# Optimization experiments

Hardware: AMD Instinct MI355X
Metric: run time of the kernel (lower is better)

The kernel has to match this reference:

```python
import jax, jax.numpy as jnp
import numpy as np

HEAD_DIM = 64
EMBED_DIM = 1024


def setup_inputs() -> dict:
    key = jax.random.key(0)
    k0, k1, k2, k3, k4, k5, k6 = jax.random.split(key, 7)
    B, T = 4, 2048
    s = 1.0 / np.sqrt(EMBED_DIM)
    return {
        "inputs": jax.random.normal(k0, (B, T, EMBED_DIM), dtype=jnp.float32),
        "Wq": jax.random.uniform(k1, (HEAD_DIM, EMBED_DIM), jnp.float32, -s, s),
        "bq": jax.random.uniform(k2, (HEAD_DIM,), jnp.float32, -s, s),
        "Wk": jax.random.uniform(k3, (HEAD_DIM, EMBED_DIM), jnp.float32, -s, s),
        "bk": jax.random.uniform(k4, (HEAD_DIM,), jnp.float32, -s, s),
        "Wv": jax.random.uniform(k5, (HEAD_DIM, EMBED_DIM), jnp.float32, -s, s),
        "bv": jax.random.uniform(k6, (HEAD_DIM,), jnp.float32, -s, s),
    }


def reference(inputs, Wq, bq, Wk, bk, Wv, bv):
    # inputs: [B, T, E]
    q = jnp.einsum("bte,he->bth", inputs, Wq) + bq  # [B, T, H]
    k = jnp.einsum("bte,he->bth", inputs, Wk) + bk
    v = jnp.einsum("bte,he->bth", inputs, Wv) + bv
    scores = jnp.einsum("bth,bsh->bts", q, k)  # [B, T, T]
    T = scores.shape[-1]
    causal = jnp.tril(jnp.ones((T, T), dtype=bool))  # True = keep
    scores = jnp.where(causal, scores, -jnp.inf)
    weights = jax.nn.softmax(scores / jnp.sqrt(jnp.float32(HEAD_DIM)), axis=-1)
    # dropout is identity in eval mode
    return jnp.einsum("bts,bsh->bth", weights, v)
```

## Files before the change

kernel.cpp:

```cpp
#include <hip/hip_runtime.h>
#include <hip/hip_bf16.h>

#define BATCH 4
#define SEQ   2048
#define EMB   1024
#define HD    64
#define BT    (BATCH * SEQ)
#define XS_STRIDE 1040

#define QSCALE 0.18033688011112042f

typedef __attribute__((ext_vector_type(8))) short bf16x8;
typedef __attribute__((ext_vector_type(4))) float f32x4;

__device__ __forceinline__ ushort f2bf(float f) {
    unsigned u = __float_as_uint(f);
    return (ushort)((u + 0x7FFFu + ((u >> 16) & 1u)) >> 16);
}

__global__ __launch_bounds__(256) void prep(
    const float* __restrict__ Wq, const float* __restrict__ bq,
    const float* __restrict__ Wk, const float* __restrict__ bk,
    const float* __restrict__ Wv, const float* __restrict__ bv,
    ushort* __restrict__ Wf, float* __restrict__ bb)
{
    const int fid = (int)blockIdx.x * 256 + (int)threadIdx.x;
    const int kc   = fid / 768;
    const int rem  = fid - kc * 768;
    const int sub  = rem >> 6;
    const int lane = rem & 63;
    const int row  = (sub & 3) * 16 + (lane & 15);
    const int e0   = kc * 32 + (lane >> 4) * 8;
    const float* W = (sub < 4) ? Wq : ((sub < 8) ? Wk : Wv);
    const float4 a0 = *(const float4*)(W + (size_t)row * EMB + e0);
    const float4 a1 = *(const float4*)(W + (size_t)row * EMB + e0 + 4);
    bf16x8 w;
    w[0] = (short)f2bf(a0.x); w[1] = (short)f2bf(a0.y);
    w[2] = (short)f2bf(a0.z); w[3] = (short)f2bf(a0.w);
    w[4] = (short)f2bf(a1.x); w[5] = (short)f2bf(a1.y);
    w[6] = (short)f2bf(a1.z); w[7] = (short)f2bf(a1.w);
    *(bf16x8*)(Wf + (size_t)fid * 8) = w;
    if (blockIdx.x == 0 && threadIdx.x < 192) {
        const int i = (int)threadIdx.x;
        const float* B = (i < 64) ? bq : ((i < 128) ? bk : bv);
        bb[i] = B[i & 63];
    }
}

__global__ __launch_bounds__(512, 2) void qkv_gemm(
    const float* __restrict__ x, const ushort* __restrict__ Wf,
    const float* __restrict__ bb,
    ushort* __restrict__ Qf, ushort* __restrict__ Kf, ushort* __restrict__ Vf)
{
    const int t0   = (int)blockIdx.x * 32;
    const int tid  = (int)threadIdx.x;
    const int wv   = tid >> 6;
    const int lane = tid & 63;
    const int col  = lane & 15, quad = lane >> 4;
    const int sg   = wv >> 1;
    const int kp   = wv & 1;
    const int sub0 = sg * 3;

    __shared__ ushort xs[32][XS_STRIDE];
    __shared__ __align__(16) float red[4][64][24];

    float4 v0[8];
    #pragma unroll
    for (int i = 0; i < 8; ++i) {
        const int idx = i * 512 + tid;
        const int row = idx >> 7, c4 = idx & 127;
        v0[i] = *(const float4*)(x + (size_t)(t0 + row) * EMB + c4 * 4);
    }
    #pragma unroll
    for (int i = 0; i < 8; ++i) {
        const int idx = i * 512 + tid;
        const int row = idx >> 7, c4 = idx & 127;
        ushort4 pk;
        pk.x = f2bf(v0[i].x); pk.y = f2bf(v0[i].y);
        pk.z = f2bf(v0[i].z); pk.w = f2bf(v0[i].w);
        *(ushort4*)&xs[row][c4 * 4] = pk;
    }
    __syncthreads();

    float4 v1[8];
    #pragma unroll
    for (int i = 0; i < 8; ++i) {
        const int idx = i * 512 + tid;
        const int row = idx >> 7, c4 = idx & 127;
        v1[i] = *(const float4*)(x + (size_t)(t0 + row) * EMB + 512 + c4 * 4);
    }

    f32x4 acc[2][3];
    #pragma unroll
    for (int rg = 0; rg < 2; ++rg)
        #pragma unroll
        for (int s = 0; s < 3; ++s) acc[rg][s] = (f32x4){0.f, 0.f, 0.f, 0.f};

    #pragma unroll 4
    for (int t = 0; t < 8; ++t) {
        const int kc = kp + 2 * t;
        const bf16x8 a0 = *(const bf16x8*)&xs[col][kc * 32 + quad * 8];
        const bf16x8 a1 = *(const bf16x8*)&xs[16 + col][kc * 32 + quad * 8];
        #pragma unroll
        for (int s = 0; s < 3; ++s) {
            const bf16x8 w = *(const bf16x8*)(Wf + ((size_t)(kc * 12 + sub0 + s) * 64 + lane) * 8);
            acc[0][s] = __builtin_amdgcn_mfma_f32_16x16x32_bf16(a0, w, acc[0][s], 0, 0, 0);
            acc[1][s] = __builtin_amdgcn_mfma_f32_16x16x32_bf16(a1, w, acc[1][s], 0, 0, 0);
        }
    }

    #pragma unroll
    for (int i = 0; i < 8; ++i) {
        const int idx = i * 512 + tid;
        const int row = idx >> 7, c4 = idx & 127;
        ushort4 pk;
        pk.x = f2bf(v1[i].x); pk.y = f2bf(v1[i].y);
        pk.z = f2bf(v1[i].z); pk.w = f2bf(v1[i].w);
        *(ushort4*)&xs[row][512 + c4 * 4] = pk;
    }
    __syncthreads();

    #pragma unroll 4
    for (int t = 0; t < 8; ++t) {
        const int kc = 16 + kp + 2 * t;
        const bf16x8 a0 = *(const bf16x8*)&xs[col][kc * 32 + quad * 8];
        const bf16x8 a1 = *(const bf16x8*)&xs[16 + col][kc * 32 + quad * 8];
        #pragma unroll
        for (int s = 0; s < 3; ++s) {
            const bf16x8 w = *(const bf16x8*)(Wf + ((size_t)(kc * 12 + sub0 + s) * 64 + lane) * 8);
            acc[0][s] = __builtin_amdgcn_mfma_f32_16x16x32_bf16(a0, w, acc[0][s], 0, 0, 0);
            acc[1][s] = __builtin_amdgcn_mfma_f32_16x16x32_bf16(a1, w, acc[1][s], 0, 0, 0);
        }
    }

    if (kp) {
        #pragma unroll
        for (int rg = 0; rg < 2; ++rg)
            #pragma unroll
            for (int s = 0; s < 3; ++s)
                *(f32x4*)&red[sg][lane][(rg * 3 + s) * 4] = acc[rg][s];
    }
    __syncthreads();
    if (kp) return;
    #pragma unroll
    for (int rg = 0; rg < 2; ++rg)
        #pragma unroll
        for (int s = 0; s < 3; ++s)
            acc[rg][s] += *(const f32x4*)&red[sg][lane][(rg * 3 + s) * 4];

    #pragma unroll
    for (int rg = 0; rg < 2; ++rg) {
        const int tt0 = t0 + rg * 16;
        const int b   = tt0 >> 11;
        const int qt  = (tt0 >> 4) & 127;
        const int sgt = tt0 + quad * 4;
        const int itk = (sgt & (SEQ - 1)) >> 6;
        #pragma unroll
        for (int s = 0; s < 3; ++s) {
            const int sub  = sub0 + s;
            const int hrow = sub * 16 + col;
            const float bias = bb[hrow];
            if (sub < 4) {
                const int h = hrow;
                const int f = h >> 5, qd = (h >> 3) & 3, jj = h & 7;
                ushort* base = Qf + (((size_t)(b * 128 + qt) * 2 + f) * 64 + qd * 16 + quad * 4) * 8 + jj;
                #pragma unroll
                for (int i = 0; i < 4; ++i)
                    base[i * 8] = f2bf((acc[rg][s][i] + bias) * QSCALE);
            } else if (sub < 8) {
                const int h = hrow - 64;
                const int f = h >> 5, qd = (h >> 3) & 3, jj = h & 7;
                const size_t frag = ((size_t)(b * 32 + itk) * 4 + ((sgt >> 4) & 3)) * 2 + f;
                ushort* base = Kf + frag * 512 + ((size_t)((sgt & 15) + 16 * qd)) * 8 + jj;
                #pragma unroll
                for (int i = 0; i < 4; ++i)
                    base[i * 8] = f2bf(acc[rg][s][i] + bias);
            } else {
                const int h = hrow - 128;
                const int k0 = sgt & 63;
                const int f = k0 >> 5, qd = (k0 >> 3) & 3, j0 = k0 & 7;
                const size_t frag = ((size_t)(b * 32 + itk) * 4 + (h >> 4)) * 2 + f;
                ushort4 pk;
                pk.x = f2bf(acc[rg][s][0] + bias); pk.y = f2bf(acc[rg][s][1] + bias);
                pk.z = f2bf(acc[rg][s][2] + bias); pk.w = f2bf(acc[rg][s][3] + bias);
                *(ushort4*)(Vf + frag * 512 + ((size_t)((h & 15) + 16 * qd)) * 8 + j0) = pk;
            }
        }
    }
}

__global__ __launch_bounds__(512, 2) void attn(
    const ushort* __restrict__ Qf, const ushort* __restrict__ Kf,
    const ushort* __restrict__ Vf, float* __restrict__ out)
{
    const int blk  = (int)blockIdx.x;
    const int b    = blk & 3;
    const int tl   = 63 - (blk >> 2);
    const int t0   = tl * 32;
    const int nt   = ((t0 + 31) >> 6) + 1;
    const int tid  = (int)threadIdx.x;
    const int j    = tid >> 6;
    const int lane = tid & 63;
    const int col  = lane & 15, quad = lane >> 4;

    const ushort* QbA = Qf + ((size_t)(b * 128 + 2 * tl) * 2) * 512;
    const bf16x8 aqA0 = *(const bf16x8*)(QbA + (size_t)lane * 8);
    const bf16x8 aqA1 = *(const bf16x8*)(QbA + 512 + (size_t)lane * 8);
    const bf16x8 aqB0 = *(const bf16x8*)(QbA + 1024 + (size_t)lane * 8);
    const bf16x8 aqB1 = *(const bf16x8*)(QbA + 1536 + (size_t)lane * 8);

    float l_a[4], l_b[4];
    f32x4 o[8];
    #pragma unroll
    for (int i = 0; i < 4; ++i) { l_a[i] = 0.f; l_b[i] = 0.f; }
    #pragma unroll
    for (int i = 0; i < 8; ++i) o[i] = (f32x4){0.f, 0.f, 0.f, 0.f};

    __shared__ ushort pt[8][32][80];
    __shared__ __align__(16) float op[8][32][68];
    __shared__ float ll[8][32];

    bf16x8 kc[4][2];
    if (j < nt) {
        const ushort* Kt = Kf + ((size_t)(b * 32 + j) * 8) * 512;
        #pragma unroll
        for (int sub = 0; sub < 4; ++sub) {
            kc[sub][0] = *(const bf16x8*)(Kt + (size_t)(sub * 2 + 0) * 512 + (size_t)lane * 8);
            kc[sub][1] = *(const bf16x8*)(Kt + (size_t)(sub * 2 + 1) * 512 + (size_t)lane * 8);
        }
    }

    for (int it = j; it < nt; it += 8) {
        const int s0 = it * 64;
        const bool hasNext = (it + 8 < nt);

        f32x4 scA[4], scB[4];
        #pragma unroll
        for (int sub = 0; sub < 4; ++sub) {
            f32x4 z = {0.f, 0.f, 0.f, 0.f};
            z = __builtin_amdgcn_mfma_f32_16x16x32_bf16(aqA0, kc[sub][0], z, 0, 0, 0);
            z = __builtin_amdgcn_mfma_f32_16x16x32_bf16(aqA1, kc[sub][1], z, 0, 0, 0);
            scA[sub] = z;
            f32x4 y = {0.f, 0.f, 0.f, 0.f};
            y = __builtin_amdgcn_mfma_f32_16x16x32_bf16(aqB0, kc[sub][0], y, 0, 0, 0);
            y = __builtin_amdgcn_mfma_f32_16x16x32_bf16(aqB1, kc[sub][1], y, 0, 0, 0);
            scB[sub] = y;
        }

        bf16x8 kn[4][2], vf[4][2];
        {
            const ushort* Vt = Vf + ((size_t)(b * 32 + it) * 8) * 512;
            #pragma unroll
            for (int sub = 0; sub < 4; ++sub) {
                vf[sub][0] = *(const bf16x8*)(Vt + (size_t)(sub * 2 + 0) * 512 + (size_t)lane * 8);
                vf[sub][1] = *(const bf16x8*)(Vt + (size_t)(sub * 2 + 1) * 512 + (size_t)lane * 8);
            }
        }
        if (hasNext) {
            const ushort* Kt = Kf + ((size_t)(b * 32 + it + 8) * 8) * 512;
            #pragma unroll
            for (int sub = 0; sub < 4; ++sub) {
                kn[sub][0] = *(const bf16x8*)(Kt + (size_t)(sub * 2 + 0) * 512 + (size_t)lane * 8);
                kn[sub][1] = *(const bf16x8*)(Kt + (size_t)(sub * 2 + 1) * 512 + (size_t)lane * 8);
            }
        }

        if (it == nt - 1) {
            #pragma unroll
            for (int sub = 0; sub < 4; ++sub)
                #pragma unroll
                for (int i = 0; i < 4; ++i) {
                    const int s  = s0 + sub * 16 + col;
                    const int tA = t0 + quad * 4 + i;
                    if (s > tA)      scA[sub][i] = -1e30f;
                    if (s > tA + 16) scB[sub][i] = -1e30f;
                }
        }

        #pragma unroll
        for (int sub = 0; sub < 4; ++sub)
            #pragma unroll
            for (int i = 0; i < 4; ++i) {
                const float pA = exp2f(scA[sub][i]);
                l_a[i] += pA;
                pt[j][quad * 4 + i][sub * 16 + col] = f2bf(pA);
                const float pB = exp2f(scB[sub][i]);
                l_b[i] += pB;
                pt[j][16 + quad * 4 + i][sub * 16 + col] = f2bf(pB);
            }

        __asm__ volatile("s_waitcnt lgkmcnt(0)" ::: "memory");
        const bf16x8 apA0 = *(const bf16x8*)&pt[j][col][quad * 8];
        const bf16x8 apA1 = *(const bf16x8*)&pt[j][col][32 + quad * 8];
        const bf16x8 apB0 = *(const bf16x8*)&pt[j][16 + col][quad * 8];
        const bf16x8 apB1 = *(const bf16x8*)&pt[j][16 + col][32 + quad * 8];

        #pragma unroll
        for (int sub = 0; sub < 4; ++sub) {
            o[sub]     = __builtin_amdgcn_mfma_f32_16x16x32_bf16(apA0, vf[sub][0], o[sub], 0, 0, 0);
            o[sub]     = __builtin_amdgcn_mfma_f32_16x16x32_bf16(apA1, vf[sub][1], o[sub], 0, 0, 0);
            o[4 + sub] = __builtin_amdgcn_mfma_f32_16x16x32_bf16(apB0, vf[sub][0], o[4 + sub], 0, 0, 0);
            o[4 + sub] = __builtin_amdgcn_mfma_f32_16x16x32_bf16(apB1, vf[sub][1], o[4 + sub], 0, 0, 0);
        }

        if (hasNext) {
            #pragma unroll
            for (int sub = 0; sub < 4; ++sub) { kc[sub][0] = kn[sub][0]; kc[sub][1] = kn[sub][1]; }
        }
    }

    #pragma unroll
    for (int d = 1; d < 16; d <<= 1)
        #pragma unroll
        for (int i = 0; i < 4; ++i) {
            l_a[i] += __shfl_xor(l_a[i], d, 64);
            l_b[i] += __shfl_xor(l_b[i], d, 64);
        }

    #pragma unroll
    for (int sub = 0; sub < 4; ++sub)
        #pragma unroll
        for (int i = 0; i < 4; ++i) {
            op[j][quad * 4 + i][sub * 16 + col]      = o[sub][i];
            op[j][16 + quad * 4 + i][sub * 16 + col] = o[4 + sub][i];
        }
    if (col == 0) {
        #pragma unroll
        for (int i = 0; i < 4; ++i) {
            ll[j][quad * 4 + i]      = l_a[i];
            ll[j][16 + quad * 4 + i] = l_b[i];
        }
    }
    __syncthreads();

    {
        const int row = tid >> 4, c0 = (tid & 15) * 4;
        float sx = 0.f, sy = 0.f, sz = 0.f, sw = 0.f, ls = 0.f;
        #pragma unroll
        for (int w = 0; w < 8; ++w) {
            const float4 p = *(const float4*)&op[w][row][c0];
            sx += p.x; sy += p.y; sz += p.z; sw += p.w;
            ls += ll[w][row];
        }
        const float rinv = 1.0f / ls;
        float4 res;
        res.x = sx * rinv; res.y = sy * rinv; res.z = sz * rinv; res.w = sw * rinv;
        *(float4*)(out + ((size_t)b * SEQ + t0 + row) * HD + c0) = res;
    }
}

extern "C" void kernel_launch(void* const* d_in, const int* in_sizes, int n_in,
                              void* d_out, int out_size, void* d_ws, size_t ws_size,
                              hipStream_t stream)
{
    const float* x  = (const float*)d_in[0];
    const float* Wq = (const float*)d_in[1];
    const float* bq = (const float*)d_in[2];
    const float* Wk = (const float*)d_in[3];
    const float* bk = (const float*)d_in[4];
    const float* Wv = (const float*)d_in[5];
    const float* bv = (const float*)d_in[6];
    float* out = (float*)d_out;

    char* ws = (char*)d_ws;
    ushort* Wf  = (ushort*)(ws);
    float*  bb  = (float*)(ws + 0x60000);
    ushort* Qfb = (ushort*)(ws + 0x61000);
    ushort* Kfb = (ushort*)(ws + 0x161000);
    ushort* Vfb = (ushort*)(ws + 0x261000);

    prep<<<96, 256, 0, stream>>>(Wq, bq, Wk, bk, Wv, bv, Wf, bb);
    qkv_gemm<<<BT / 32, 512, 0, stream>>>(x, Wf, bb, Qfb, Kfb, Vfb);
    attn<<<256, 512, 0, stream>>>(Qfb, Kfb, Vfb, out);
}
```

Baseline: 105.1 us.

## Split attention into 64-row query tiles with causal KV chunking and atomic combine

The attention kernel now gives each block 64 query rows instead of 32. The key range is split into chunks of up to 8 KV tiles, spread over 320 blocks, and each warp handles exactly one KV tile. Partial outputs and row sums go to a workspace, and the last-arriving block for each query tile, found with an atomic counter, combines them. The goal is to balance the causal triangle across blocks and to double Q reuse per K/V load, at the cost of a large shared buffer (about 136KB, which limits occupancy to one block per CU), extra global partial traffic, and the loss of the K prefetch loop.

Result: slower. 208.2 us (+98.1%).

```diff
diff --git a/kernel.cpp b/kernel.cpp
--- a/kernel.cpp
+++ b/kernel.cpp
@@ -22,7 +22,7 @@
     const float* __restrict__ Wq, const float* __restrict__ bq,
     const float* __restrict__ Wk, const float* __restrict__ bk,
     const float* __restrict__ Wv, const float* __restrict__ bv,
-    ushort* __restrict__ Wf, float* __restrict__ bb)
+    ushort* __restrict__ Wf, float* __restrict__ bb, uint* __restrict__ cnt)
 {
     const int fid = (int)blockIdx.x * 256 + (int)threadIdx.x;
     const int kc   = fid / 768;
@@ -45,6 +45,7 @@
         const float* B = (i < 64) ? bq : ((i < 128) ? bk : bv);
         bb[i] = B[i & 63];
     }
+    if (blockIdx.x == 1 && threadIdx.x < 128) cnt[threadIdx.x] = 0u;
 }
 
 __global__ __launch_bounds__(512, 2) void qkv_gemm(
@@ -191,161 +192,185 @@
 
 __global__ __launch_bounds__(512, 2) void attn(
     const ushort* __restrict__ Qf, const ushort* __restrict__ Kf,
-    const ushort* __restrict__ Vf, float* __restrict__ out)
+    const ushort* __restrict__ Vf, float* __restrict__ part,
+    uint* __restrict__ cnt, float* __restrict__ out)
 {
-    const int blk  = (int)blockIdx.x;
-    const int b    = blk & 3;
-    const int tl   = 63 - (blk >> 2);
-    const int t0   = tl * 32;
-    const int nt   = ((t0 + 31) >> 6) + 1;
+    const int u = (int)blockIdx.x;
+    int b, tl, chunk, chunks;
+    if (u < 128)      { const int q = u >> 2;                   b = q >> 3; tl = 24 + (q & 7); chunk = u & 3;     chunks = 4; }
+    else if (u < 224) { const int v = u - 128; const int q = v / 3; b = q >> 3; tl = 16 + (q & 7); chunk = v - q * 3; chunks = 3; }
+    else if (u < 288) { const int v = u - 224; const int q = v >> 1; b = q >> 3; tl = 8 + (q & 7);  chunk = v & 1;     chunks = 2; }
+    else              { const int v = u - 288;                  b = v >> 3; tl = v & 7;        chunk = 0;         chunks = 1; }
+
+    const int t0   = tl * 64;
+    const int nt   = tl + 1;
     const int tid  = (int)threadIdx.x;
     const int j    = tid >> 6;
     const int lane = tid & 63;
     const int col  = lane & 15, quad = lane >> 4;
-
-    const ushort* QbA = Qf + ((size_t)(b * 128 + 2 * tl) * 2) * 512;
-    const bf16x8 aqA0 = *(const bf16x8*)(QbA + (size_t)lane * 8);
-    const bf16x8 aqA1 = *(const bf16x8*)(QbA + 512 + (size_t)lane * 8);
-    const bf16x8 aqB0 = *(const bf16x8*)(QbA + 1024 + (size_t)lane * 8);
-    const bf16x8 aqB1 = *(const bf16x8*)(QbA + 1536 + (size_t)lane * 8);
-
-    float l_a[4], l_b[4];
-    f32x4 o[8];
-    #pragma unroll
-    for (int i = 0; i < 4; ++i) { l_a[i] = 0.f; l_b[i] = 0.f; }
-    #pragma unroll
-    for (int i = 0; i < 8; ++i) o[i] = (f32x4){0.f, 0.f, 0.f, 0.f};
-
-    __shared__ ushort pt[8][32][80];
-    __shared__ __align__(16) float op[8][32][68];
-    __shared__ float ll[8][32];
-
-    bf16x8 kc[4][2];
-    if (j < nt) {
-        const ushort* Kt = Kf + ((size_t)(b * 32 + j) * 8) * 512;
+    const int it   = chunk * 8 + j;
+    const bool active = (it < nt);
+
+    __shared__ __align__(16) char smem[139264];
+    ushort (*pt)[64][80] = (ushort (*)[64][80])smem;
+    float  (*op)[64][68] = (float  (*)[64][68])smem;
+    __shared__ float ll[8][64];
+    __shared__ int flag;
+
+    f32x4 o[4][4];
+    float l_r[16];
+    #pragma unroll
+    for (int qs = 0; qs < 4; ++qs)
+        #pragma unroll
+        for (int d = 0; d < 4; ++d) o[qs][d] = (f32x4){0.f, 0.f, 0.f, 0.f};
+    #pragma unroll
+    for (int k = 0; k < 16; ++k) l_r[k] = 0.f;
+
+    if (active) {
+        const ushort* Qb = Qf + ((size_t)(b * 128 + tl * 4) * 2) * 512;
+        bf16x8 aq[4][2];
+        #pragma unroll
+        for (int qs = 0; qs < 4; ++qs) {
+            aq[qs][0] = *(const bf16x8*)(Qb + (size_t)(qs * 2 + 0) * 512 + (size_t)lane * 8);
+            aq[qs][1] = *(const bf16x8*)(Qb + (size_t)(qs * 2 + 1) * 512 + (size_t)lane * 8);
+        }
+        const ushort* Kt = Kf + ((size_t)(b * 32 + it) * 8) * 512;
+        bf16x8 kc[4][2];
         #pragma unroll
         for (int sub = 0; sub < 4; ++sub) {
             kc[sub][0] = *(const bf16x8*)(Kt + (size_t)(sub * 2 + 0) * 512 + (size_t)lane * 8);
             kc[sub][1] = *(const bf16x8*)(Kt + (size_t)(sub * 2 + 1) * 512 + (size_t)lane * 8);
         }
-    }
-
-    for (int it = j; it < nt; it += 8) {
+        const ushort* Vt = Vf + ((size_t)(b * 32 + it) * 8) * 512;
+        bf16x8 vf[4][2];
+        #pragma unroll
+        for (int sub = 0; sub < 4; ++sub) {
+            vf[sub][0] = *(const bf16x8*)(Vt + (size_t)(sub * 2 + 0) * 512 + (size_t)lane * 8);
+            vf[sub][1] = *(const bf16x8*)(Vt + (size_t)(sub * 2 + 1) * 512 + (size_t)lane * 8);
+        }
+
         const int s0 = it * 64;
-        const bool hasNext = (it + 8 < nt);
-
-        f32x4 scA[4], scB[4];
-        #pragma unroll
-        for (int sub = 0; sub < 4; ++sub) {
-            f32x4 z = {0.f, 0.f, 0.f, 0.f};
-            z = __builtin_amdgcn_mfma_f32_16x16x32_bf16(aqA0, kc[sub][0], z, 0, 0, 0);
-            z = __builtin_amdgcn_mfma_f32_16x16x32_bf16(aqA1, kc[sub][1], z, 0, 0, 0);
-            scA[sub] = z;
-            f32x4 y = {0.f, 0.f, 0.f, 0.f};
-            y = __builtin_amdgcn_mfma_f32_16x16x32_bf16(aqB0, kc[sub][0], y, 0, 0, 0);
-            y = __builtin_amdgcn_mfma_f32_16x16x32_bf16(aqB1, kc[sub][1], y, 0, 0, 0);
-            scB[sub] = y;
-        }
-
-        bf16x8 kn[4][2], vf[4][2];
-        {
-            const ushort* Vt = Vf + ((size_t)(b * 32 + it) * 8) * 512;
+        const bool diag = (it == nt - 1);
+
+        #pragma unroll
+        for (int qs = 0; qs < 4; ++qs) {
+            f32x4 sc[4];
             #pragma unroll
             for (int sub = 0; sub < 4; ++sub) {
-                vf[sub][0] = *(const bf16x8*)(Vt + (size_t)(sub * 2 + 0) * 512 + (size_t)lane * 8);
-                vf[sub][1] = *(const bf16x8*)(Vt + (size_t)(sub * 2 + 1) * 512 + (size_t)lane * 8);
+                f32x4 z = {0.f, 0.f, 0.f, 0.f};
+                z = __builtin_amdgcn_mfma_f32_16x16x32_bf16(aq[qs][0], kc[sub][0], z, 0, 0, 0);
+                z = __builtin_amdgcn_mfma_f32_16x16x32_bf16(aq[qs][1], kc[sub][1], z, 0, 0, 0);
+                sc[sub] = z;
             }
-        }
-        if (hasNext) {
-            const ushort* Kt = Kf + ((size_t)(b * 32 + it + 8) * 8) * 512;
-            #pragma unroll
-            for (int sub = 0; sub < 4; ++sub) {
-                kn[sub][0] = *(const bf16x8*)(Kt + (size_t)(sub * 2 + 0) * 512 + (size_t)lane * 8);
-                kn[sub][1] = *(const bf16x8*)(Kt + (size_t)(sub * 2 + 1) * 512 + (size_t)lane * 8);
+            if (diag) {
+                #pragma unroll
+                for (int sub = 0; sub < 4; ++sub)
+                    #pragma unroll
+                    for (int i = 0; i < 4; ++i) {
+                        const int s = s0 + sub * 16 + col;
+                        const int t = t0 + qs * 16 + quad * 4 + i;
+                        if (s > t) sc[sub][i] = -1e30f;
+                    }
             }
-        }
-
-        if (it == nt - 1) {
             #pragma unroll
             for (int sub = 0; sub < 4; ++sub)
                 #pragma unroll
                 for (int i = 0; i < 4; ++i) {
-                    const int s  = s0 + sub * 16 + col;
-                    const int tA = t0 + quad * 4 + i;
-                    if (s > tA)      scA[sub][i] = -1e30f;
-                    if (s > tA + 16) scB[sub][i] = -1e30f;
+                    const float p = exp2f(sc[sub][i]);
+                    l_r[qs * 4 + i] += p;
+                    pt[j][qs * 16 + quad * 4 + i][sub * 16 + col] = f2bf(p);
                 }
         }
 
-        #pragma unroll
-        for (int sub = 0; sub < 4; ++sub)
-            #pragma unroll
-            for (int i = 0; i < 4; ++i) {
-                const float pA = exp2f(scA[sub][i]);
-                l_a[i] += pA;
-                pt[j][quad * 4 + i][sub * 16 + col] = f2bf(pA);
-                const float pB = exp2f(scB[sub][i]);
-                l_b[i] += pB;
-                pt[j][16 + quad * 4 + i][sub * 16 + col] = f2bf(pB);
+        __asm__ volatile("s_waitcnt lgkmcnt(0)" ::: "memory");
+        #pragma unroll
+        for (int qs = 0; qs < 4; ++qs) {
+            const bf16x8 ap0 = *(const bf16x8*)&pt[j][qs * 16 + col][quad * 8];
+            const bf16x8 ap1 = *(const bf16x8*)&pt[j][qs * 16 + col][32 + quad * 8];
+            #pragma unroll
+            for (int d = 0; d < 4; ++d) {
+                o[qs][d] = __builtin_amdgcn_mfma_f32_16x16x32_bf16(ap0, vf[d][0], o[qs][d], 0, 0, 0);
+                o[qs][d] = __builtin_amdgcn_mfma_f32_16x16x32_bf16(ap1, vf[d][1], o[qs][d], 0, 0, 0);
             }
-
-        __asm__ volatile("s_waitcnt lgkmcnt(0)" ::: "memory");
-        const bf16x8 apA0 = *(const bf16x8*)&pt[j][col][quad * 8];
-        const bf16x8 apA1 = *(const bf16x8*)&pt[j][col][32 + quad * 8];
-        const bf16x8 apB0 = *(const bf16x8*)&pt[j][16 + col][quad * 8];
-        const bf16x8 apB1 = *(const bf16x8*)&pt[j][16 + col][32 + quad * 8];
-
-        #pragma unroll
-        for (int sub = 0; sub < 4; ++sub) {
-            o[sub]     = __builtin_amdgcn_mfma_f32_16x16x32_bf16(apA0, vf[sub][0], o[sub], 0, 0, 0);
-            o[sub]     = __builtin_amdgcn_mfma_f32_16x16x32_bf16(apA1, vf[sub][1], o[sub], 0, 0, 0);
-            o[4 + sub] = __builtin_amdgcn_mfma_f32_16x16x32_bf16(apB0, vf[sub][0], o[4 + sub], 0, 0, 0);
-            o[4 + sub] = __builtin_amdgcn_mfma_f32_16x16x32_bf16(apB1, vf[sub][1], o[4 + sub], 0, 0, 0);
-        }
-
-        if (hasNext) {
-            #pragma unroll
-            for (int sub = 0; sub < 4; ++sub) { kc[sub][0] = kn[sub][0]; kc[sub][1] = kn[sub][1]; }
         }
     }
 
     #pragma unroll
     for (int d = 1; d < 16; d <<= 1)
         #pragma unroll
-        for (int i = 0; i < 4; ++i) {
-            l_a[i] += __shfl_xor(l_a[i], d, 64);
-            l_b[i] += __shfl_xor(l_b[i], d, 64);
-        }
-
-    #pragma unroll
-    for (int sub = 0; sub < 4; ++sub)
-        #pragma unroll
-        for (int i = 0; i < 4; ++i) {
-            op[j][quad * 4 + i][sub * 16 + col]      = o[sub][i];
-            op[j][16 + quad * 4 + i][sub * 16 + col] = o[4 + sub][i];
-        }
+        for (int k = 0; k < 16; ++k) l_r[k] += __shfl_xor(l_r[k], d, 64);
+
+    __syncthreads();
+
+    #pragma unroll
+    for (int qs = 0; qs < 4; ++qs)
+        #pragma unroll
+        for (int d = 0; d < 4; ++d)
+            #pragma unroll
+            for (int i = 0; i < 4; ++i)
+                op[j][qs * 16 + quad * 4 + i][d * 16 + col] = o[qs][d][i];
     if (col == 0) {
         #pragma unroll
-        for (int i = 0; i < 4; ++i) {
-            ll[j][quad * 4 + i]      = l_a[i];
-            ll[j][16 + quad * 4 + i] = l_b[i];
-        }
+        for (int qs = 0; qs < 4; ++qs)
+            #pragma unroll
+            for (int i = 0; i < 4; ++i)
+                ll[j][qs * 16 + quad * 4 + i] = l_r[qs * 4 + i];
     }
     __syncthreads();
 
-    {
-        const int row = tid >> 4, c0 = (tid & 15) * 4;
-        float sx = 0.f, sy = 0.f, sz = 0.f, sw = 0.f, ls = 0.f;
-        #pragma unroll
-        for (int w = 0; w < 8; ++w) {
-            const float4 p = *(const float4*)&op[w][row][c0];
-            sx += p.x; sy += p.y; sz += p.z; sw += p.w;
-            ls += ll[w][row];
-        }
+    const int row = tid >> 3, c0 = (tid & 7) * 8;
+    float acc[8];
+    #pragma unroll
+    for (int c = 0; c < 8; ++c) acc[c] = 0.f;
+    float ls = 0.f;
+    #pragma unroll
+    for (int w = 0; w < 8; ++w) {
+        #pragma unroll
+        for (int c = 0; c < 8; ++c) acc[c] += op[w][row][c0 + c];
+        ls += ll[w][row];
+    }
+
+    if (chunks == 1) {
         const float rinv = 1.0f / ls;
-        float4 res;
-        res.x = sx * rinv; res.y = sy * rinv; res.z = sz * rinv; res.w = sw * rinv;
-        *(float4*)(out + ((size_t)b * SEQ + t0 + row) * HD + c0) = res;
+        float4 r0, r1;
+        r0.x = acc[0] * rinv; r0.y = acc[1] * rinv; r0.z = acc[2] * rinv; r0.w = acc[3] * rinv;
+        r1.x = acc[4] * rinv; r1.y = acc[5] * rinv; r1.z = acc[6] * rinv; r1.w = acc[7] * rinv;
+        float* dst = out + ((size_t)b * SEQ + t0 + row) * HD + c0;
+        *(float4*)dst = r0; *(float4*)(dst + 4) = r1;
+    } else {
+        float* slot = part + (size_t)u * 4160;
+        *(float4*)(slot + row * 64 + c0)     = (float4){acc[0], acc[1], acc[2], acc[3]};
+        *(float4*)(slot + row * 64 + c0 + 4) = (float4){acc[4], acc[5], acc[6], acc[7]};
+        if ((tid & 7) == 0) slot[4096 + row] = ls;
+        __threadfence();
+        __syncthreads();
+        if (tid == 0) flag = (int)atomicAdd(&cnt[b * 32 + tl], 1u);
+        __syncthreads();
+        if (flag == chunks - 1) {
+            __threadfence();
+            int base;
+            if (tl >= 24)      base = 4 * ((b << 3) + (tl - 24));
+            else if (tl >= 16) base = 128 + 3 * ((b << 3) + (tl - 16));
+            else               base = 224 + 2 * ((b << 3) + (tl - 8));
+            float fa[8];
+            #pragma unroll
+            for (int c = 0; c < 8; ++c) fa[c] = 0.f;
+            float fls = 0.f;
+            for (int cc = 0; cc < chunks; ++cc) {
+                const float* s2 = part + (size_t)(base + cc) * 4160;
+                const float4 p0 = *(const float4*)(s2 + row * 64 + c0);
+                const float4 p1 = *(const float4*)(s2 + row * 64 + c0 + 4);
+                fa[0] += p0.x; fa[1] += p0.y; fa[2] += p0.z; fa[3] += p0.w;
+                fa[4] += p1.x; fa[5] += p1.y; fa[6] += p1.z; fa[7] += p1.w;
+                fls += s2[4096 + row];
+            }
+            const float rinv = 1.0f / fls;
+            float4 r0, r1;
+            r0.x = fa[0] * rinv; r0.y = fa[1] * rinv; r0.z = fa[2] * rinv; r0.w = fa[3] * rinv;
+            r1.x = fa[4] * rinv; r1.y = fa[5] * rinv; r1.z = fa[6] * rinv; r1.w = fa[7] * rinv;
+            float* dst = out + ((size_t)b * SEQ + t0 + row) * HD + c0;
+            *(float4*)dst = r0; *(float4*)(dst + 4) = r1;
+        }
     }
 }
 
@@ -363,13 +388,15 @@
     float* out = (float*)d_out;
 
     char* ws = (char*)d_ws;
-    ushort* Wf  = (ushort*)(ws);
-    float*  bb  = (float*)(ws + 0x60000);
-    ushort* Qfb = (ushort*)(ws + 0x61000);
-    ushort* Kfb = (ushort*)(ws + 0x161000);
-    ushort* Vfb = (ushort*)(ws + 0x261000);
-
-    prep<<<96, 256, 0, stream>>>(Wq, bq, Wk, bk, Wv, bv, Wf, bb);
+    ushort* Wf   = (ushort*)(ws);
+    float*  bb   = (float*)(ws + 0x60000);
+    uint*   cnt  = (uint*)(ws + 0x60400);
+    ushort* Qfb  = (ushort*)(ws + 0x61000);
+    ushort* Kfb  = (ushort*)(ws + 0x161000);
+    ushort* Vfb  = (ushort*)(ws + 0x261000);
+    float*  part = (float*)(ws + 0x361000);
+
+    prep<<<96, 256, 0, stream>>>(Wq, bq, Wk, bk, Wv, bv, Wf, bb, cnt);
     qkv_gemm<<<BT / 32, 512, 0, stream>>>(x, Wf, bb, Qfb, Kfb, Vfb);
-    attn<<<256, 512, 0, stream>>>(Qfb, Kfb, Vfb, out);
+    attn<<<320, 512, 0, stream>>>(Qfb, Kfb, Vfb, part, cnt, out);
 }
```
